# Kernel tuning notes

Hardware: AMD Instinct MI355X
Metric: run time of the kernel (lower is better)

Reference implementation:

```python
import jax, jax.numpy as jnp
import numpy as np

N_NODES = 100000
N_EDGES = 1600000
F_IN = 128
F_EDGE = 16
HID = 64


def gcn_conv(x, W, b, src, dst, n):
    # PyG GCNConv: add self-loops, symmetric normalization D^-1/2 (A+I) D^-1/2
    h = x @ W  # [N, out]
    loop = jnp.arange(n, dtype=src.dtype)
    src_f = jnp.concatenate([src, loop])
    dst_f = jnp.concatenate([dst, loop])
    ones = jnp.ones(src_f.shape[0], dtype=h.dtype)
    deg = jax.ops.segment_sum(ones, dst_f, num_segments=n)
    dinv = jnp.where(deg > 0, jax.lax.rsqrt(deg), 0.0)
    norm = dinv[src_f] * dinv[dst_f]  # [E+N]
    msg = h[src_f] * norm[:, None]
    out = jax.ops.segment_sum(msg, dst_f, num_segments=n)
    return out + b


def setup_inputs() -> dict:
    key = jax.random.key(0)
    ks = jax.random.split(key, 16)
    g = lambda k, shape, fan_in: jax.random.normal(k, shape, dtype=jnp.float32) * (1.0 / np.sqrt(fan_in))
    inp = {
        "x": jax.random.normal(ks[0], (N_NODES, F_IN), dtype=jnp.float32),
        "edge_index": jax.random.randint(ks[1], (2, N_EDGES), 0, N_NODES, dtype=jnp.int64) if jax.config.read('jax_enable_x64') else jax.random.randint(ks[1], (2, N_EDGES), 0, N_NODES, dtype=jnp.int32),
        "edge_attr": jax.random.normal(ks[2], (N_EDGES, F_EDGE), dtype=jnp.float32),
        # GCN layers
        "W1": g(ks[3], (F_IN, HID), F_IN), "b1": jnp.zeros((HID,), jnp.float32),
        "W2": g(ks[4], (HID, HID), HID), "b2": jnp.zeros((HID,), jnp.float32),
        "W3": g(ks[5], (HID, HID), HID), "b3": jnp.zeros((HID,), jnp.float32),
        # edge MLP: Linear(2*HID+F_EDGE -> HID), Linear(HID -> 32), Linear(32 -> 2)
        "Wm1": g(ks[6], (2 * HID + F_EDGE, HID), 2 * HID + F_EDGE), "bm1": jnp.zeros((HID,), jnp.float32),
        "Wm2": g(ks[7], (HID, 32), HID), "bm2": jnp.zeros((32,), jnp.float32),
        "Wm3": g(ks[8], (32, 2), 32), "bm3": jnp.zeros((2,), jnp.float32),
    }
    return inp


def reference(x, edge_index, edge_attr, W1, b1, W2, b2, W3, b3, Wm1, bm1, Wm2, bm2, Wm3, bm3):
    src, dst = edge_index[0], edge_index[1]
    n = x.shape[0]
    h = jax.nn.relu(gcn_conv(x, W1, b1, src, dst, n))
    h = jax.nn.relu(gcn_conv(h, W2, b2, src, dst, n))
    h = jax.nn.relu(gcn_conv(h, W3, b3, src, dst, n))
    # edge classifier: gather endpoints, concat edge features, small MLP (eval mode -> no dropout)
    e = jnp.concatenate([h[src], h[dst], edge_attr], axis=1)  # [E, 2*HID+F_EDGE]
    e = jax.nn.relu(e @ Wm1 + bm1)
    e = jax.nn.relu(e @ Wm2 + bm2)
    return e @ Wm3 + bm3  # [E, 2]
```

## Files before the change

### kernel.cpp

```cpp
#include <hip/hip_runtime.h>

typedef __attribute__((ext_vector_type(8))) short bf16x8;
typedef __attribute__((ext_vector_type(4))) float f32x4;
typedef __attribute__((ext_vector_type(4))) unsigned int u32x4;

__device__ __forceinline__ short f2bf(float f) {
  unsigned u = __float_as_uint(f);
  u = (u + 0x7fffu + ((u >> 16) & 1u)) >> 16;
  return (short)u;
}
__device__ __forceinline__ float bf2f(unsigned short u) {
  return __uint_as_float(((unsigned)u) << 16);
}
__device__ __forceinline__ unsigned cvtpk(float lo, float hi) {
  unsigned r;
  asm("v_cvt_pk_bf16_f32 %0, %1, %2" : "=v"(r) : "v"(lo), "v"(hi));
  return r;
}
__device__ __forceinline__ bf16x8 u2b(u32x4 w) {
  union { u32x4 u; bf16x8 b; } x; x.u = w; return x.b;
}

#define FILLB 2048
#define PACKB 40

__global__ __launch_bounds__(256) void prep_k(
    const float* __restrict__ x, const float* __restrict__ W1,
    const float* __restrict__ Wm1, const float* __restrict__ Wm2,
    const int* __restrict__ src, const int* __restrict__ dst,
    unsigned* cursor, int* __restrict__ csr_pad,
    short* __restrict__ We1p, short* __restrict__ We2p,
    unsigned short* __restrict__ lin, int e, int n, int nNodeB)
{
  __shared__ __align__(16) short Wl[8192];
  const int tid = threadIdx.x;

  if (blockIdx.x < FILLB) {
    const int part  = blockIdx.x & 7;
    const int lo    = (int)(((long)n * part) >> 3);
    const int hi    = (int)(((long)n * (part + 1)) >> 3);
    const int brank = blockIdx.x >> 3;
    const long stride = (long)(FILLB >> 3) * 256;
    const int e4 = e >> 2;
    const int4* dst4 = (const int4*)dst;
    for (long i = (long)brank * 256 + tid; i < e4; i += stride) {
      int4 d = dst4[i];
      long eb = i * 4;
      if (d.x >= lo && d.x < hi) { int p = (int)atomicAdd(&cursor[d.x], 1u); if (p < 64) csr_pad[((size_t)d.x << 6) + p] = src[eb]; }
      if (d.y >= lo && d.y < hi) { int p = (int)atomicAdd(&cursor[d.y], 1u); if (p < 64) csr_pad[((size_t)d.y << 6) + p] = src[eb + 1]; }
      if (d.z >= lo && d.z < hi) { int p = (int)atomicAdd(&cursor[d.z], 1u); if (p < 64) csr_pad[((size_t)d.z << 6) + p] = src[eb + 2]; }
      if (d.w >= lo && d.w < hi) { int p = (int)atomicAdd(&cursor[d.w], 1u); if (p < 64) csr_pad[((size_t)d.w << 6) + p] = src[eb + 3]; }
    }
    for (long i = (long)e4 * 4 + (long)brank * 256 + tid; i < e; i += stride) {
      int d = dst[i];
      if (d >= lo && d < hi) { int p = (int)atomicAdd(&cursor[d], 1u); if (p < 64) csr_pad[((size_t)d << 6) + p] = src[i]; }
    }
  } else if (blockIdx.x < FILLB + nNodeB) {
    const int nb = blockIdx.x - FILLB;
    for (int i = tid; i < 8192; i += 256) {
      int j = i & 7, l = (i >> 3) & 63, c = (i >> 9) & 3, kk = i >> 11;
      int row = kk * 32 + ((l >> 4) * 8) + j, col = c * 16 + (l & 15);
      Wl[i] = f2bf(W1[row * 64 + col]);
    }
    __syncthreads();
    const int lane = tid & 63;
    const int wid  = tid >> 6;
    const int g    = lane >> 4;
    const int r16  = lane & 15;
    const int base = nb * 64 + wid * 16;
    if (base < n) {
      int arow = base + r16;
      if (arow >= n) arow = n - 1;
      const bf16x8* wb = (const bf16x8*)Wl;
      f32x4 acc[4];
      #pragma unroll
      for (int c = 0; c < 4; ++c) acc[c] = (f32x4){0.f, 0.f, 0.f, 0.f};
      #pragma unroll
      for (int kk = 0; kk < 4; ++kk) {
        const float4* af = (const float4*)(x + (size_t)arow * 128 + kk * 32 + 8 * g);
        float4 u = af[0], v = af[1];
        u32x4 w;
        w[0] = cvtpk(u.x, u.y); w[1] = cvtpk(u.z, u.w);
        w[2] = cvtpk(v.x, v.y); w[3] = cvtpk(v.z, v.w);
        bf16x8 a = u2b(w);
        #pragma unroll
        for (int c = 0; c < 4; ++c)
          acc[c] = __builtin_amdgcn_mfma_f32_16x16x32_bf16(a, wb[(kk * 4 + c) * 64 + lane], acc[c], 0, 0, 0);
      }
      #pragma unroll
      for (int rr = 0; rr < 4; ++rr) {
        int orow = base + g * 4 + rr;
        if (orow < n) {
          unsigned short* cp = lin + (size_t)orow * 64 + r16;
          cp[0]  = (unsigned short)f2bf(acc[0][rr]);
          cp[16] = (unsigned short)f2bf(acc[1][rr]);
          cp[32] = (unsigned short)f2bf(acc[2][rr]);
          cp[48] = (unsigned short)f2bf(acc[3][rr]);
        }
      }
    }
  } else {
    const int t = (blockIdx.x - FILLB - nNodeB) * 256 + tid;
    const int stride = PACKB * 256;
    for (int i = t; i < 10240; i += stride) {
      int j = i & 7, l = (i >> 3) & 63, c = (i >> 9) & 3, kk = i >> 11;
      int row = kk * 32 + ((l >> 4) * 8) + j;
      int r_ = l & 15;
      int col = 32 * (c >> 1) + 8 * (r_ >> 2) + 4 * (c & 1) + (r_ & 3);
      We1p[i] = f2bf(row < 144 ? Wm1[row * 64 + col] : 0.f);
    }
    for (int i = t; i < 2048; i += stride) {
      int j = i & 7, l = (i >> 3) & 63, c = (i >> 9) & 1, kk = (i >> 10) & 1;
      int row = kk * 32 + ((l >> 4) * 8) + j, col = c * 16 + (l & 15);
      We2p[i] = f2bf(Wm2[row * 32 + col]);
    }
  }
}

__global__ __launch_bounds__(256) void agg_csr_k(
    const unsigned short* __restrict__ lin, const unsigned* __restrict__ deg,
    const int* __restrict__ csr_pad, const float* __restrict__ bias,
    unsigned short* __restrict__ out, int n)
{
  const int node = blockIdx.x * 4 + (threadIdx.x >> 6);
  if (node >= n) return;
  const int lane = threadIdx.x & 63;
  const int es = lane >> 4;
  const int fq = lane & 15;
  const float dn = rsqrtf((float)(deg[node] + 1u));
  const int cnt = (int)deg[node];
  const int* sp = csr_pad + ((size_t)node << 6);
  float ax = 0.f, ay = 0.f, az = 0.f, aw = 0.f;
  if (es == 0) {
    ushort4 v = *(const ushort4*)(lin + (size_t)node * 64 + fq * 4);
    float w = dn * dn;
    ax = w * bf2f(v.x); ay = w * bf2f(v.y); az = w * bf2f(v.z); aw = w * bf2f(v.w);
  }
  #pragma unroll 4
  for (int j = es; j < cnt; j += 4) {
    int s = sp[j];
    float w = rsqrtf((float)(deg[s] + 1u)) * dn;
    ushort4 v = *(const ushort4*)(lin + (size_t)s * 64 + fq * 4);
    ax += w * bf2f(v.x); ay += w * bf2f(v.y);
    az += w * bf2f(v.z); aw += w * bf2f(v.w);
  }
  ax += __shfl_xor(ax, 16, 64); ax += __shfl_xor(ax, 32, 64);
  ay += __shfl_xor(ay, 16, 64); ay += __shfl_xor(ay, 32, 64);
  az += __shfl_xor(az, 16, 64); az += __shfl_xor(az, 32, 64);
  aw += __shfl_xor(aw, 16, 64); aw += __shfl_xor(aw, 32, 64);
  if (es == 0) {
    float4 b = *(const float4*)(bias + fq * 4);
    ushort4 o;
    o.x = (unsigned short)f2bf(fmaxf(ax + b.x, 0.f));
    o.y = (unsigned short)f2bf(fmaxf(ay + b.y, 0.f));
    o.z = (unsigned short)f2bf(fmaxf(az + b.z, 0.f));
    o.w = (unsigned short)f2bf(fmaxf(aw + b.w, 0.f));
    *(ushort4*)(out + (size_t)node * 64 + fq * 4) = o;
  }
}

__global__ __launch_bounds__(256) void agg_gemm_k(
    const unsigned short* __restrict__ h_in, const unsigned* __restrict__ deg,
    const int* __restrict__ csr_pad, const float* __restrict__ W,
    const float* __restrict__ bias, unsigned short* __restrict__ h_out, int n)
{
  __shared__ __align__(16) short Wl[4096];
  __shared__ __align__(16) short X[4][16][72];
  const int tid = threadIdx.x;
  for (int i = tid; i < 4096; i += 256) {
    int j = i & 7, l = (i >> 3) & 63, c = (i >> 9) & 3, kk = i >> 11;
    int row = kk * 32 + ((l >> 4) * 8) + j, col = c * 16 + (l & 15);
    Wl[i] = f2bf(W[row * 64 + col]);
  }
  const int lane = tid & 63;
  const int wid  = tid >> 6;
  const int es   = lane >> 4;
  const int fq   = lane & 15;
  const int base = blockIdx.x * 64 + wid * 16;

  for (int nd = 0; nd < 16; ++nd) {
    int node = base + nd;
    if (node >= n) node = n - 1;
    const float dn = rsqrtf((float)(deg[node] + 1u));
    const int cnt = (int)deg[node];
    const int* sp = csr_pad + ((size_t)node << 6);
    float ax = 0.f, ay = 0.f, az = 0.f, aw = 0.f;
    if (es == 0) {
      ushort4 v = *(const ushort4*)(h_in + (size_t)node * 64 + fq * 4);
      float w = dn * dn;
      ax = w * bf2f(v.x); ay = w * bf2f(v.y); az = w * bf2f(v.z); aw = w * bf2f(v.w);
    }
    #pragma unroll 4
    for (int j = es; j < cnt; j += 4) {
      int s = sp[j];
      float w = rsqrtf((float)(deg[s] + 1u)) * dn;
      ushort4 v = *(const ushort4*)(h_in + (size_t)s * 64 + fq * 4);
      ax += w * bf2f(v.x); ay += w * bf2f(v.y);
      az += w * bf2f(v.z); aw += w * bf2f(v.w);
    }
    ax += __shfl_xor(ax, 16, 64); ax += __shfl_xor(ax, 32, 64);
    ay += __shfl_xor(ay, 16, 64); ay += __shfl_xor(ay, 32, 64);
    az += __shfl_xor(az, 16, 64); az += __shfl_xor(az, 32, 64);
    aw += __shfl_xor(aw, 16, 64); aw += __shfl_xor(aw, 32, 64);
    if (es == 0) {
      ushort4 o;
      o.x = (unsigned short)f2bf(ax); o.y = (unsigned short)f2bf(ay);
      o.z = (unsigned short)f2bf(az); o.w = (unsigned short)f2bf(aw);
      *(ushort4*)&X[wid][nd][fq * 4] = o;
    }
  }
  __syncthreads();

  const int g = es, r16 = fq;
  float bcol[4];
  #pragma unroll
  for (int c = 0; c < 4; ++c) bcol[c] = bias[c * 16 + r16];
  const bf16x8* wb = (const bf16x8*)Wl;
  f32x4 acc[4];
  #pragma unroll
  for (int c = 0; c < 4; ++c) acc[c] = (f32x4){bcol[c], bcol[c], bcol[c], bcol[c]};
  #pragma unroll
  for (int kk = 0; kk < 2; ++kk) {
    bf16x8 a = *(const bf16x8*)&X[wid][r16][kk * 32 + 8 * g];
    #pragma unroll
    for (int c = 0; c < 4; ++c)
      acc[c] = __builtin_amdgcn_mfma_f32_16x16x32_bf16(a, wb[(kk * 4 + c) * 64 + lane], acc[c], 0, 0, 0);
  }
  #pragma unroll
  for (int rr = 0; rr < 4; ++rr) {
    int orow = base + g * 4 + rr;
    if (orow < n) {
      unsigned short* cp = h_out + (size_t)orow * 64 + r16;
      cp[0]  = (unsigned short)f2bf(fmaxf(acc[0][rr], 0.f));
      cp[16] = (unsigned short)f2bf(fmaxf(acc[1][rr], 0.f));
      cp[32] = (unsigned short)f2bf(fmaxf(acc[2][rr], 0.f));
      cp[48] = (unsigned short)f2bf(fmaxf(acc[3][rr], 0.f));
    }
  }
}

__global__ __launch_bounds__(256) void edge_mlp_mfma_k(
    const unsigned short* __restrict__ hb, const float* __restrict__ ea,
    const int* __restrict__ src, const int* __restrict__ dst,
    const short* __restrict__ W1p, const short* __restrict__ W2p,
    const float* __restrict__ bm1, const float* __restrict__ bm2,
    const float* __restrict__ Wm3, const float* __restrict__ bm3,
    float* __restrict__ out, int E, int ntiles)
{
  const int tid  = threadIdx.x;
  const int lane = tid & 63;
  const int wid  = tid >> 6;
  const int g    = lane >> 4;
  const int r16  = lane & 15;

  bf16x8 w1f[20];
  #pragma unroll
  for (int t = 0; t < 20; ++t) w1f[t] = ((const bf16x8*)W1p)[t * 64 + lane];
  bf16x8 w2f[4];
  #pragma unroll
  for (int t = 0; t < 4; ++t) w2f[t] = ((const bf16x8*)W2p)[t * 64 + lane];

  f32x4 b1v[4];
  #pragma unroll
  for (int c = 0; c < 4; ++c) {
    float4 v = *(const float4*)(bm1 + 32 * (c >> 1) + 8 * g + 4 * (c & 1));
    b1v[c] = (f32x4){v.x, v.y, v.z, v.w};
  }
  f32x4 b2v[2];
  #pragma unroll
  for (int c = 0; c < 2; ++c) {
    float4 v = *(const float4*)(bm2 + c * 16 + 4 * g);
    b2v[c] = (f32x4){v.x, v.y, v.z, v.w};
  }
  float4 w3a[2], w3b[2];
  #pragma unroll
  for (int c = 0; c < 2; ++c) {
    w3a[c] = *(const float4*)(Wm3 + (c * 16 + 4 * g) * 2);
    w3b[c] = *(const float4*)(Wm3 + (c * 16 + 4 * g) * 2 + 4);
  }
  const float b30 = bm3[0], b31 = bm3[1];

  const int ngroups = (ntiles + 3) >> 2;
  if (blockIdx.x >= ngroups) return;

  int mye1, sl1, dl1;
  bf16x8 c_a0, c_a1, c_a2, c_a3;
  float4 c_e0, c_e1;
  {
    int e = (blockIdx.x * 4 + wid) * 16 + r16;
    int mye = (e < E) ? e : (E - 1);
    int sl = src[mye], dl = dst[mye];
    const bf16x8* hs = (const bf16x8*)(hb + (size_t)sl * 64);
    c_a0 = hs[g]; c_a1 = hs[4 + g];
    const bf16x8* hd = (const bf16x8*)(hb + (size_t)dl * 64);
    c_a2 = hd[g]; c_a3 = hd[4 + g];
    if (g < 2) {
      const float4* ep = (const float4*)(ea + (size_t)mye * 16 + 8 * g);
      c_e0 = ep[0]; c_e1 = ep[1];
    }
    int grp1 = blockIdx.x + gridDim.x;
    if (grp1 > ngroups - 1) grp1 = ngroups - 1;
    int e1 = (grp1 * 4 + wid) * 16 + r16;
    mye1 = (e1 < E) ? e1 : (E - 1);
    sl1 = src[mye1]; dl1 = dst[mye1];
  }

  for (int grp = blockIdx.x; grp < ngroups; grp += gridDim.x) {
    const int e0 = (grp * 4 + wid) * 16;

    bf16x8 n_a0, n_a1, n_a2, n_a3;
    float4 n_e0, n_e1;
    {
      const bf16x8* hs = (const bf16x8*)(hb + (size_t)sl1 * 64);
      n_a0 = hs[g]; n_a1 = hs[4 + g];
      const bf16x8* hd = (const bf16x8*)(hb + (size_t)dl1 * 64);
      n_a2 = hd[g]; n_a3 = hd[4 + g];
      if (g < 2) {
        const float4* ep = (const float4*)(ea + (size_t)mye1 * 16 + 8 * g);
        n_e0 = ep[0]; n_e1 = ep[1];
      }
    }
    int mye2, sl2, dl2;
    {
      int grp2 = grp + 2 * gridDim.x;
      if (grp2 > ngroups - 1) grp2 = ngroups - 1;
      int e2 = (grp2 * 4 + wid) * 16 + r16;
      mye2 = (e2 < E) ? e2 : (E - 1);
      sl2 = src[mye2]; dl2 = dst[mye2];
    }

    bf16x8 a4;
    if (g < 2) {
      u32x4 w;
      w[0] = cvtpk(c_e0.x, c_e0.y); w[1] = cvtpk(c_e0.z, c_e0.w);
      w[2] = cvtpk(c_e1.x, c_e1.y); w[3] = cvtpk(c_e1.z, c_e1.w);
      a4 = u2b(w);
    } else {
      a4 = (bf16x8){0, 0, 0, 0, 0, 0, 0, 0};
    }

    f32x4 acc[4];
    #pragma unroll
    for (int c = 0; c < 4; ++c) acc[c] = b1v[c];
    #pragma unroll
    for (int c = 0; c < 4; ++c) {
      acc[c] = __builtin_amdgcn_mfma_f32_16x16x32_bf16(w1f[0 * 4 + c], c_a0, acc[c], 0, 0, 0);
      acc[c] = __builtin_amdgcn_mfma_f32_16x16x32_bf16(w1f[1 * 4 + c], c_a1, acc[c], 0, 0, 0);
      acc[c] = __builtin_amdgcn_mfma_f32_16x16x32_bf16(w1f[2 * 4 + c], c_a2, acc[c], 0, 0, 0);
      acc[c] = __builtin_amdgcn_mfma_f32_16x16x32_bf16(w1f[3 * 4 + c], c_a3, acc[c], 0, 0, 0);
      acc[c] = __builtin_amdgcn_mfma_f32_16x16x32_bf16(w1f[4 * 4 + c], a4,   acc[c], 0, 0, 0);
    }

    u32x4 x0w, x1w;
    x0w[0] = cvtpk(fmaxf(acc[0][0], 0.f), fmaxf(acc[0][1], 0.f));
    x0w[1] = cvtpk(fmaxf(acc[0][2], 0.f), fmaxf(acc[0][3], 0.f));
    x0w[2] = cvtpk(fmaxf(acc[1][0], 0.f), fmaxf(acc[1][1], 0.f));
    x0w[3] = cvtpk(fmaxf(acc[1][2], 0.f), fmaxf(acc[1][3], 0.f));
    x1w[0] = cvtpk(fmaxf(acc[2][0], 0.f), fmaxf(acc[2][1], 0.f));
    x1w[1] = cvtpk(fmaxf(acc[2][2], 0.f), fmaxf(acc[2][3], 0.f));
    x1w[2] = cvtpk(fmaxf(acc[3][0], 0.f), fmaxf(acc[3][1], 0.f));
    x1w[3] = cvtpk(fmaxf(acc[3][2], 0.f), fmaxf(acc[3][3], 0.f));
    bf16x8 xa0 = u2b(x0w), xa1 = u2b(x1w);

    f32x4 acc2[2];
    #pragma unroll
    for (int c = 0; c < 2; ++c) acc2[c] = b2v[c];
    #pragma unroll
    for (int c = 0; c < 2; ++c) {
      acc2[c] = __builtin_amdgcn_mfma_f32_16x16x32_bf16(w2f[0 * 2 + c], xa0, acc2[c], 0, 0, 0);
      acc2[c] = __builtin_amdgcn_mfma_f32_16x16x32_bf16(w2f[1 * 2 + c], xa1, acc2[c], 0, 0, 0);
    }

    float p0 = 0.f, p1 = 0.f;
    #pragma unroll
    for (int c = 0; c < 2; ++c) {
      float v0 = fmaxf(acc2[c][0], 0.f);
      float v1 = fmaxf(acc2[c][1], 0.f);
      float v2 = fmaxf(acc2[c][2], 0.f);
      float v3 = fmaxf(acc2[c][3], 0.f);
      p0 = fmaf(v0, w3a[c].x, p0); p1 = fmaf(v0, w3a[c].y, p1);
      p0 = fmaf(v1, w3a[c].z, p0); p1 = fmaf(v1, w3a[c].w, p1);
      p0 = fmaf(v2, w3b[c].x, p0); p1 = fmaf(v2, w3b[c].y, p1);
      p0 = fmaf(v3, w3b[c].z, p0); p1 = fmaf(v3, w3b[c].w, p1);
    }
    p0 += __shfl_xor(p0, 16, 64); p0 += __shfl_xor(p0, 32, 64);
    p1 += __shfl_xor(p1, 16, 64); p1 += __shfl_xor(p1, 32, 64);
    if (g == 0) {
      int e = e0 + r16;
      if (e < E) {
        float2 o; o.x = p0 + b30; o.y = p1 + b31;
        *(float2*)(out + (size_t)e * 2) = o;
      }
    }

    c_a0 = n_a0; c_a1 = n_a1; c_a2 = n_a2; c_a3 = n_a3;
    c_e0 = n_e0; c_e1 = n_e1;
    mye1 = mye2; sl1 = sl2; dl1 = dl2;
  }
}

extern "C" void kernel_launch(void* const* d_in, const int* in_sizes, int n_in,
                              void* d_out, int out_size, void* d_ws, size_t ws_size,
                              hipStream_t stream) {
  const float* x   = (const float*)d_in[0];
  const int*   ei  = (const int*)d_in[1];
  const float* ea  = (const float*)d_in[2];
  const float* W1  = (const float*)d_in[3];
  const float* b1  = (const float*)d_in[4];
  const float* W2  = (const float*)d_in[5];
  const float* b2  = (const float*)d_in[6];
  const float* W3  = (const float*)d_in[7];
  const float* b3  = (const float*)d_in[8];
  const float* Wm1 = (const float*)d_in[9];
  const float* bm1 = (const float*)d_in[10];
  const float* Wm2 = (const float*)d_in[11];
  const float* bm2 = (const float*)d_in[12];
  const float* Wm3 = (const float*)d_in[13];
  const float* bm3 = (const float*)d_in[14];

  const int N  = in_sizes[0] / 128;
  const int E  = in_sizes[1] / 2;
  const int* srcp = ei;
  const int* dstp = ei + E;

  float* ws = (float*)d_ws;
  size_t off = 0;
  unsigned* cursor  = (unsigned*)(ws + off);  off += (size_t)N;
  int*      csr_pad = (int*)(ws + off);       off += (size_t)N * 64;
  unsigned short* lin = (unsigned short*)(ws + off); off += (size_t)N * 32;
  unsigned short* hA  = (unsigned short*)(ws + off); off += (size_t)N * 32;
  unsigned short* hB  = (unsigned short*)(ws + off); off += (size_t)N * 32;
  short* We1p = (short*)(ws + off); off += 5120;
  short* We2p = (short*)(ws + off); off += 1024;

  const int gNode = (N + 63) / 64;
  const int gAgg  = (N + 3) / 4;
  const int ntiles = (E + 15) / 16;

  hipMemsetAsync(cursor, 0, (size_t)N * 4, stream);

  prep_k<<<FILLB + gNode + PACKB, 256, 0, stream>>>(
      x, W1, Wm1, Wm2, srcp, dstp, cursor, csr_pad, We1p, We2p, lin, E, N, gNode);

  agg_csr_k<<<gAgg, 256, 0, stream>>>(lin, cursor, csr_pad, b1, hA, N);
  agg_gemm_k<<<gNode, 256, 0, stream>>>(hA, cursor, csr_pad, W2, b2, hB, N);
  agg_gemm_k<<<gNode, 256, 0, stream>>>(hB, cursor, csr_pad, W3, b3, hA, N);

  edge_mlp_mfma_k<<<2048, 256, 0, stream>>>(hA, ea, srcp, dstp, We1p, We2p,
      bm1, bm2, Wm3, bm3, (float*)d_out, E, ntiles);
}
```

Before: 363.2 us.

## Pre-scale node features by dinv to drop per-edge degree gathers in aggregation

The ReLU output of each GCN layer is pre-multiplied by its own D^-1/2 factor when stored, so the gather loops in layers 2 and 3 only sum neighbor rows and apply the destination dinv once. This removes a random deg[s] load and an rsqrt per edge from the two agg_gemm passes. The fused prep kernel is also split into separate fill, pack and node-GEMM launches. The split adds launch overhead and loses the overlap the combined kernel gave, and the change affects bf16 rounding. Layer 1's agg_csr_k still computes per-edge weights from deg[s].

```diff
diff --git a/kernel.cpp b/kernel.cpp
--- a/kernel.cpp
+++ b/kernel.cpp
@@ -21,98 +21,95 @@
   union { u32x4 u; bf16x8 b; } x; x.u = w; return x.b;
 }
 
-#define FILLB 2048
-#define PACKB 40
-
-__global__ __launch_bounds__(256) void prep_k(
+__global__ __launch_bounds__(256) void fill_pad_k(const int* __restrict__ src,
+                                                  const int* __restrict__ dst,
+                                                  unsigned* cursor,
+                                                  int* __restrict__ csr_pad, int e, int n) {
+  const int part  = blockIdx.x & 7;
+  const int lo    = (int)(((long)n * part) >> 3);
+  const int hi    = (int)(((long)n * (part + 1)) >> 3);
+  const int nb    = gridDim.x >> 3;
+  const int brank = blockIdx.x >> 3;
+  const long stride = (long)nb * 256;
+  const int e4 = e >> 2;
+  const int4* dst4 = (const int4*)dst;
+  for (long i = (long)brank * 256 + threadIdx.x; i < e4; i += stride) {
+    int4 d = dst4[i];
+    long eb = i * 4;
+    if (d.x >= lo && d.x < hi) { int p = (int)atomicAdd(&cursor[d.x], 1u); if (p < 64) csr_pad[((size_t)d.x << 6) + p] = src[eb]; }
+    if (d.y >= lo && d.y < hi) { int p = (int)atomicAdd(&cursor[d.y], 1u); if (p < 64) csr_pad[((size_t)d.y << 6) + p] = src[eb + 1]; }
+    if (d.z >= lo && d.z < hi) { int p = (int)atomicAdd(&cursor[d.z], 1u); if (p < 64) csr_pad[((size_t)d.z << 6) + p] = src[eb + 2]; }
+    if (d.w >= lo && d.w < hi) { int p = (int)atomicAdd(&cursor[d.w], 1u); if (p < 64) csr_pad[((size_t)d.w << 6) + p] = src[eb + 3]; }
+  }
+  for (long i = (long)e4 * 4 + (long)brank * 256 + threadIdx.x; i < e; i += stride) {
+    int d = dst[i];
+    if (d >= lo && d < hi) { int p = (int)atomicAdd(&cursor[d], 1u); if (p < 64) csr_pad[((size_t)d << 6) + p] = src[i]; }
+  }
+}
+
+__global__ void pack_edge_k(const float* __restrict__ Wm1, const float* __restrict__ Wm2,
+                            short* __restrict__ We1p, short* __restrict__ We2p) {
+  const int t = blockIdx.x * 256 + threadIdx.x;
+  const int stride = gridDim.x * 256;
+  for (int i = t; i < 10240; i += stride) {
+    int j = i & 7, l = (i >> 3) & 63, c = (i >> 9) & 3, kk = i >> 11;
+    int row = kk * 32 + ((l >> 4) * 8) + j;
+    int r_ = l & 15;
+    int col = 32 * (c >> 1) + 8 * (r_ >> 2) + 4 * (c & 1) + (r_ & 3);
+    We1p[i] = f2bf(row < 144 ? Wm1[row * 64 + col] : 0.f);
+  }
+  for (int i = t; i < 2048; i += stride) {
+    int j = i & 7, l = (i >> 3) & 63, c = (i >> 9) & 1, kk = (i >> 10) & 1;
+    int row = kk * 32 + ((l >> 4) * 8) + j, col = c * 16 + (l & 15);
+    We2p[i] = f2bf(Wm2[row * 32 + col]);
+  }
+}
+
+__global__ __launch_bounds__(256) void node_mfma_k(
     const float* __restrict__ x, const float* __restrict__ W1,
-    const float* __restrict__ Wm1, const float* __restrict__ Wm2,
-    const int* __restrict__ src, const int* __restrict__ dst,
-    unsigned* cursor, int* __restrict__ csr_pad,
-    short* __restrict__ We1p, short* __restrict__ We2p,
-    unsigned short* __restrict__ lin, int e, int n, int nNodeB)
+    unsigned short* __restrict__ lin, int n)
 {
   __shared__ __align__(16) short Wl[8192];
   const int tid = threadIdx.x;
-
-  if (blockIdx.x < FILLB) {
-    const int part  = blockIdx.x & 7;
-    const int lo    = (int)(((long)n * part) >> 3);
-    const int hi    = (int)(((long)n * (part + 1)) >> 3);
-    const int brank = blockIdx.x >> 3;
-    const long stride = (long)(FILLB >> 3) * 256;
-    const int e4 = e >> 2;
-    const int4* dst4 = (const int4*)dst;
-    for (long i = (long)brank * 256 + tid; i < e4; i += stride) {
-      int4 d = dst4[i];
-      long eb = i * 4;
-      if (d.x >= lo && d.x < hi) { int p = (int)atomicAdd(&cursor[d.x], 1u); if (p < 64) csr_pad[((size_t)d.x << 6) + p] = src[eb]; }
-      if (d.y >= lo && d.y < hi) { int p = (int)atomicAdd(&cursor[d.y], 1u); if (p < 64) csr_pad[((size_t)d.y << 6) + p] = src[eb + 1]; }
-      if (d.z >= lo && d.z < hi) { int p = (int)atomicAdd(&cursor[d.z], 1u); if (p < 64) csr_pad[((size_t)d.z << 6) + p] = src[eb + 2]; }
-      if (d.w >= lo && d.w < hi) { int p = (int)atomicAdd(&cursor[d.w], 1u); if (p < 64) csr_pad[((size_t)d.w << 6) + p] = src[eb + 3]; }
-    }
-    for (long i = (long)e4 * 4 + (long)brank * 256 + tid; i < e; i += stride) {
-      int d = dst[i];
-      if (d >= lo && d < hi) { int p = (int)atomicAdd(&cursor[d], 1u); if (p < 64) csr_pad[((size_t)d << 6) + p] = src[i]; }
-    }
-  } else if (blockIdx.x < FILLB + nNodeB) {
-    const int nb = blockIdx.x - FILLB;
-    for (int i = tid; i < 8192; i += 256) {
-      int j = i & 7, l = (i >> 3) & 63, c = (i >> 9) & 3, kk = i >> 11;
-      int row = kk * 32 + ((l >> 4) * 8) + j, col = c * 16 + (l & 15);
-      Wl[i] = f2bf(W1[row * 64 + col]);
-    }
-    __syncthreads();
-    const int lane = tid & 63;
-    const int wid  = tid >> 6;
-    const int g    = lane >> 4;
-    const int r16  = lane & 15;
-    const int base = nb * 64 + wid * 16;
-    if (base < n) {
-      int arow = base + r16;
-      if (arow >= n) arow = n - 1;
-      const bf16x8* wb = (const bf16x8*)Wl;
-      f32x4 acc[4];
-      #pragma unroll
-      for (int c = 0; c < 4; ++c) acc[c] = (f32x4){0.f, 0.f, 0.f, 0.f};
-      #pragma unroll
-      for (int kk = 0; kk < 4; ++kk) {
-        const float4* af = (const float4*)(x + (size_t)arow * 128 + kk * 32 + 8 * g);
-        float4 u = af[0], v = af[1];
-        u32x4 w;
-        w[0] = cvtpk(u.x, u.y); w[1] = cvtpk(u.z, u.w);
-        w[2] = cvtpk(v.x, v.y); w[3] = cvtpk(v.z, v.w);
-        bf16x8 a = u2b(w);
-        #pragma unroll
-        for (int c = 0; c < 4; ++c)
-          acc[c] = __builtin_amdgcn_mfma_f32_16x16x32_bf16(a, wb[(kk * 4 + c) * 64 + lane], acc[c], 0, 0, 0);
-      }
-      #pragma unroll
-      for (int rr = 0; rr < 4; ++rr) {
-        int orow = base + g * 4 + rr;
-        if (orow < n) {
-          unsigned short* cp = lin + (size_t)orow * 64 + r16;
-          cp[0]  = (unsigned short)f2bf(acc[0][rr]);
-          cp[16] = (unsigned short)f2bf(acc[1][rr]);
-          cp[32] = (unsigned short)f2bf(acc[2][rr]);
-          cp[48] = (unsigned short)f2bf(acc[3][rr]);
-        }
-      }
-    }
-  } else {
-    const int t = (blockIdx.x - FILLB - nNodeB) * 256 + tid;
-    const int stride = PACKB * 256;
-    for (int i = t; i < 10240; i += stride) {
-      int j = i & 7, l = (i >> 3) & 63, c = (i >> 9) & 3, kk = i >> 11;
-      int row = kk * 32 + ((l >> 4) * 8) + j;
-      int r_ = l & 15;
-      int col = 32 * (c >> 1) + 8 * (r_ >> 2) + 4 * (c & 1) + (r_ & 3);
-      We1p[i] = f2bf(row < 144 ? Wm1[row * 64 + col] : 0.f);
-    }
-    for (int i = t; i < 2048; i += stride) {
-      int j = i & 7, l = (i >> 3) & 63, c = (i >> 9) & 1, kk = (i >> 10) & 1;
-      int row = kk * 32 + ((l >> 4) * 8) + j, col = c * 16 + (l & 15);
-      We2p[i] = f2bf(Wm2[row * 32 + col]);
+  for (int i = tid; i < 8192; i += 256) {
+    int j = i & 7, l = (i >> 3) & 63, c = (i >> 9) & 3, kk = i >> 11;
+    int row = kk * 32 + ((l >> 4) * 8) + j, col = c * 16 + (l & 15);
+    Wl[i] = f2bf(W1[row * 64 + col]);
+  }
+  __syncthreads();
+  const int lane = tid & 63;
+  const int wid  = tid >> 6;
+  const int g    = lane >> 4;
+  const int r16  = lane & 15;
+  const int base = blockIdx.x * 64 + wid * 16;
+  if (base >= n) return;
+  int arow = base + r16;
+  if (arow >= n) arow = n - 1;
+  const bf16x8* wb = (const bf16x8*)Wl;
+  f32x4 acc[4];
+  #pragma unroll
+  for (int c = 0; c < 4; ++c) acc[c] = (f32x4){0.f, 0.f, 0.f, 0.f};
+  #pragma unroll
+  for (int kk = 0; kk < 4; ++kk) {
+    const float4* af = (const float4*)(x + (size_t)arow * 128 + kk * 32 + 8 * g);
+    float4 u = af[0], v = af[1];
+    u32x4 w;
+    w[0] = cvtpk(u.x, u.y); w[1] = cvtpk(u.z, u.w);
+    w[2] = cvtpk(v.x, v.y); w[3] = cvtpk(v.z, v.w);
+    bf16x8 a = u2b(w);
+    #pragma unroll
+    for (int c = 0; c < 4; ++c)
+      acc[c] = __builtin_amdgcn_mfma_f32_16x16x32_bf16(a, wb[(kk * 4 + c) * 64 + lane], acc[c], 0, 0, 0);
+  }
+  #pragma unroll
+  for (int rr = 0; rr < 4; ++rr) {
+    int orow = base + g * 4 + rr;
+    if (orow < n) {
+      unsigned short* cp = lin + (size_t)orow * 64 + r16;
+      cp[0]  = (unsigned short)f2bf(acc[0][rr]);
+      cp[16] = (unsigned short)f2bf(acc[1][rr]);
+      cp[32] = (unsigned short)f2bf(acc[2][rr]);
+      cp[48] = (unsigned short)f2bf(acc[3][rr]);
     }
   }
 }
@@ -151,14 +148,15 @@
   if (es == 0) {
     float4 b = *(const float4*)(bias + fq * 4);
     ushort4 o;
-    o.x = (unsigned short)f2bf(fmaxf(ax + b.x, 0.f));
-    o.y = (unsigned short)f2bf(fmaxf(ay + b.y, 0.f));
-    o.z = (unsigned short)f2bf(fmaxf(az + b.z, 0.f));
-    o.w = (unsigned short)f2bf(fmaxf(aw + b.w, 0.f));
+    o.x = (unsigned short)f2bf(fmaxf(ax + b.x, 0.f) * dn);
+    o.y = (unsigned short)f2bf(fmaxf(ay + b.y, 0.f) * dn);
+    o.z = (unsigned short)f2bf(fmaxf(az + b.z, 0.f) * dn);
+    o.w = (unsigned short)f2bf(fmaxf(aw + b.w, 0.f) * dn);
     *(ushort4*)(out + (size_t)node * 64 + fq * 4) = o;
   }
 }
 
+template<int SCALE_OUT>
 __global__ __launch_bounds__(256) void agg_gemm_k(
     const unsigned short* __restrict__ h_in, const unsigned* __restrict__ deg,
     const int* __restrict__ csr_pad, const float* __restrict__ W,
@@ -187,16 +185,14 @@
     float ax = 0.f, ay = 0.f, az = 0.f, aw = 0.f;
     if (es == 0) {
       ushort4 v = *(const ushort4*)(h_in + (size_t)node * 64 + fq * 4);
-      float w = dn * dn;
-      ax = w * bf2f(v.x); ay = w * bf2f(v.y); az = w * bf2f(v.z); aw = w * bf2f(v.w);
+      ax = bf2f(v.x); ay = bf2f(v.y); az = bf2f(v.z); aw = bf2f(v.w);
     }
     #pragma unroll 4
     for (int j = es; j < cnt; j += 4) {
       int s = sp[j];
-      float w = rsqrtf((float)(deg[s] + 1u)) * dn;
       ushort4 v = *(const ushort4*)(h_in + (size_t)s * 64 + fq * 4);
-      ax += w * bf2f(v.x); ay += w * bf2f(v.y);
-      az += w * bf2f(v.z); aw += w * bf2f(v.w);
+      ax += bf2f(v.x); ay += bf2f(v.y);
+      az += bf2f(v.z); aw += bf2f(v.w);
     }
     ax += __shfl_xor(ax, 16, 64); ax += __shfl_xor(ax, 32, 64);
     ay += __shfl_xor(ay, 16, 64); ay += __shfl_xor(ay, 32, 64);
@@ -204,8 +200,8 @@
     aw += __shfl_xor(aw, 16, 64); aw += __shfl_xor(aw, 32, 64);
     if (es == 0) {
       ushort4 o;
-      o.x = (unsigned short)f2bf(ax); o.y = (unsigned short)f2bf(ay);
-      o.z = (unsigned short)f2bf(az); o.w = (unsigned short)f2bf(aw);
+      o.x = (unsigned short)f2bf(ax * dn); o.y = (unsigned short)f2bf(ay * dn);
+      o.z = (unsigned short)f2bf(az * dn); o.w = (unsigned short)f2bf(aw * dn);
       *(ushort4*)&X[wid][nd][fq * 4] = o;
     }
   }
@@ -230,11 +226,12 @@
   for (int rr = 0; rr < 4; ++rr) {
     int orow = base + g * 4 + rr;
     if (orow < n) {
+      float so = SCALE_OUT ? rsqrtf((float)(deg[orow] + 1u)) : 1.f;
       unsigned short* cp = h_out + (size_t)orow * 64 + r16;
-      cp[0]  = (unsigned short)f2bf(fmaxf(acc[0][rr], 0.f));
-      cp[16] = (unsigned short)f2bf(fmaxf(acc[1][rr], 0.f));
-      cp[32] = (unsigned short)f2bf(fmaxf(acc[2][rr], 0.f));
-      cp[48] = (unsigned short)f2bf(fmaxf(acc[3][rr], 0.f));
+      cp[0]  = (unsigned short)f2bf(fmaxf(acc[0][rr], 0.f) * so);
+      cp[16] = (unsigned short)f2bf(fmaxf(acc[1][rr], 0.f) * so);
+      cp[32] = (unsigned short)f2bf(fmaxf(acc[2][rr], 0.f) * so);
+      cp[48] = (unsigned short)f2bf(fmaxf(acc[3][rr], 0.f) * so);
     }
   }
 }
@@ -437,14 +434,15 @@
   const int gAgg  = (N + 3) / 4;
   const int ntiles = (E + 15) / 16;
 
-  hipMemsetAsync(cursor, 0, (size_t)N * 4, stream);
-
-  prep_k<<<FILLB + gNode + PACKB, 256, 0, stream>>>(
-      x, W1, Wm1, Wm2, srcp, dstp, cursor, csr_pad, We1p, We2p, lin, E, N, gNode);
-
+  (void)hipMemsetAsync(cursor, 0, (size_t)N * 4, stream);
+
+  fill_pad_k<<<2048, 256, 0, stream>>>(srcp, dstp, cursor, csr_pad, E, N);
+  pack_edge_k<<<40, 256, 0, stream>>>(Wm1, Wm2, We1p, We2p);
+
+  node_mfma_k<<<gNode, 256, 0, stream>>>(x, W1, lin, N);
   agg_csr_k<<<gAgg, 256, 0, stream>>>(lin, cursor, csr_pad, b1, hA, N);
-  agg_gemm_k<<<gNode, 256, 0, stream>>>(hA, cursor, csr_pad, W2, b2, hB, N);
-  agg_gemm_k<<<gNode, 256, 0, stream>>>(hB, cursor, csr_pad, W3, b3, hA, N);
+  agg_gemm_k<1><<<gNode, 256, 0, stream>>>(hA, cursor, csr_pad, W2, b2, hB, N);
+  agg_gemm_k<0><<<gNode, 256, 0, stream>>>(hB, cursor, csr_pad, W3, b3, hA, N);
 
   edge_mlp_mfma_k<<<2048, 256, 0, stream>>>(hA, ea, srcp, dstp, We1p, We2p,
       bm1, bm2, Wm3, bm3, (float*)d_out, E, ntiles);
```

Result: no change. 357.5 us (-1.6%).
